# Optimization experiments

Hardware: AMD Instinct MI355X
Metric: run time of the kernel (lower is better)

Reference implementation:

```python
import jax, jax.numpy as jnp
import numpy as np

T = 2048        # Tmax encoder frames
EPROJS = 1024   # encoder projection dim (Henc)
DUNITS = 512    # prediction net hidden
EMBED = 512     # embedding dim
JOINT = 512     # joint space dim
ODIM = 10000    # output vocab
BLANK = 0


def setup_inputs() -> dict:
    key = jax.random.key(0)
    ks = jax.random.split(key, 11)
    def g(k, shape, scale):
        return (jax.random.normal(k, shape, dtype=jnp.float32) * scale)
    inp = {
        'h': jax.random.normal(ks[0], (T, EPROJS), dtype=jnp.float32),
        # Embedding with padding_idx=blank -> blank row zeroed
        'embed': g(ks[1], (ODIM, EMBED), 0.05).at[BLANK].set(0.0),
        # LSTMCell params (torch gate order: i, f, g, o)
        'W_ih': g(ks[2], (4 * DUNITS, EMBED), 1.0 / np.sqrt(EMBED)),
        'W_hh': g(ks[3], (4 * DUNITS, DUNITS), 1.0 / np.sqrt(DUNITS)),
        'b_ih': g(ks[4], (4 * DUNITS,), 0.01),
        'b_hh': g(ks[5], (4 * DUNITS,), 0.01),
        # joint network
        'W_enc': g(ks[6], (JOINT, EPROJS), 1.0 / np.sqrt(EPROJS)),
        'b_enc': g(ks[7], (JOINT,), 0.01),
        'W_dec': g(ks[8], (JOINT, DUNITS), 1.0 / np.sqrt(DUNITS)),  # no bias
        'W_out': g(ks[9], (ODIM, JOINT), 1.0 / np.sqrt(JOINT)),
        'b_out': g(ks[10], (ODIM,), 0.01),
    }
    return inp


def _lstm_cell(x, h_prev, c_prev, W_ih, W_hh, b_ih, b_hh):
    gates = W_ih @ x + b_ih + W_hh @ h_prev + b_hh  # (4*DUNITS,)
    i, f, g, o = jnp.split(gates, 4)
    c = jax.nn.sigmoid(f) * c_prev + jax.nn.sigmoid(i) * jnp.tanh(g)
    h = jax.nn.sigmoid(o) * jnp.tanh(c)
    return h, c


def reference(h, embed, W_ih, W_hh, b_ih, b_hh, W_enc, b_enc, W_dec, W_out, b_out):
    # Precompute encoder-side joint projection (same math, hoisted out of loop)
    h_proj = h @ W_enc.T + b_enc  # (T, JOINT)

    # Initial prediction-net step on zero embedding from zero state
    zeros_e = jnp.zeros((EMBED,), dtype=h.dtype)
    zeros_d = jnp.zeros((DUNITS,), dtype=h.dtype)
    y0, c0 = _lstm_cell(zeros_e, zeros_d, zeros_d, W_ih, W_hh, b_ih, b_hh)

    def step(carry, hp_t):
        y, c, score = carry
        # joint: tanh(lin_enc(h_t) + lin_dec(y)) -> lin_out -> log_softmax
        ytu = jax.nn.log_softmax(W_out @ jnp.tanh(hp_t + W_dec @ y) + b_out)
        logp = jnp.max(ytu)
        pred = jnp.argmax(ytu)
        emitted = pred != BLANK
        # Candidate prediction-net update with embedded token
        ey = embed[pred]
        y_new, c_new = _lstm_cell(ey, y, c, W_ih, W_hh, b_ih, b_hh)
        y = jnp.where(emitted, y_new, y)
        c = jnp.where(emitted, c_new, c)
        score = score + jnp.where(emitted, logp, jnp.zeros_like(logp))
        tok = jnp.where(emitted, pred, BLANK).astype(jnp.int32)
        return (y, c, score), tok

    (y, c, score), yseq = jax.lax.scan(step, (y0, c0, jnp.float32(0.0)), h_proj)
    # yseq: (T,) int32, BLANK where no symbol was emitted at that frame
    return yseq, score
```

## Files before the change

kernel.cpp:

```cpp
#include <hip/hip_runtime.h>
#include <stdint.h>

typedef unsigned long long u64;
typedef uint32_t u32;

#define NB     256
#define NT     256
#define TMAX   2048
#define EPROJS 1024
#define DUNITS 512
#define EMBED  512
#define JOINT  512
#define ODIM   10000

#define N_LSTM 32
#define CONS0  32
#define N_CONS 223
#define AGG_B  255
#define MAGIC  0xD07ED07Eu

#define WS_PK   0
#define WS_SA   7168
#define WS_DN   14336
#define WS_Y    15360
#define WS_U    23552
#define WS_HP   32768

__device__ __forceinline__ float aloadf(const float* p){
  return __hip_atomic_load(p, __ATOMIC_RELAXED, __HIP_MEMORY_SCOPE_AGENT);
}
__device__ __forceinline__ void astoref(float* p, float v){
  __hip_atomic_store(p, v, __ATOMIC_RELAXED, __HIP_MEMORY_SCOPE_AGENT);
}
__device__ __forceinline__ u64 aloadu64(const u64* p){
  return __hip_atomic_load(p, __ATOMIC_RELAXED, __HIP_MEMORY_SCOPE_AGENT);
}
__device__ __forceinline__ void astoreu64(u64* p, u64 v){
  __hip_atomic_store(p, v, __ATOMIC_RELAXED, __HIP_MEMORY_SCOPE_AGENT);
}
__device__ __forceinline__ u32 aloadu32(const u32* p){
  return __hip_atomic_load(p, __ATOMIC_RELAXED, __HIP_MEMORY_SCOPE_AGENT);
}
__device__ __forceinline__ void astoreu32(u32* p, u32 v){
  __hip_atomic_store(p, v, __ATOMIC_RELAXED, __HIP_MEMORY_SCOPE_AGENT);
}

__device__ __forceinline__ u32 ordbits(float f){
  u32 u = __float_as_uint(f);
  return (u & 0x80000000u) ? ~u : (u | 0x80000000u);
}
__device__ __forceinline__ float unordbits(u32 o){
  u32 u = (o & 0x80000000u) ? (o & 0x7fffffffu) : ~o;
  return __uint_as_float(u);
}
__device__ __forceinline__ float sigmoidf_(float x){ return 1.0f/(1.0f+expf(-x)); }

__device__ __forceinline__ float wredsum(float v){
  #pragma unroll
  for (int o=32;o>0;o>>=1) v += __shfl_xor(v, o);
  return v;
}
__device__ __forceinline__ u64 wredmax64(u64 v){
  #pragma unroll
  for (int o=32;o>0;o>>=1){ u64 x = __shfl_xor(v, o); v = (x>v)?x:v; }
  return v;
}

__device__ __forceinline__ int zslot(int j){
  return (j&7)*64 + ((j>>3) ^ ((j&7)<<2));
}

#define LOAD8(dst, baseptr) { const float4* _p=(const float4*)(baseptr); \
  float4 _a=_p[0], _b=_p[1]; \
  dst[0]=_a.x; dst[1]=_a.y; dst[2]=_a.z; dst[3]=_a.w; \
  dst[4]=_b.x; dst[5]=_b.y; dst[6]=_b.z; dst[7]=_b.w; }

__global__ void rnnt_init(char* ws){
  u32* p = (u32*)ws;
  for (int i = threadIdx.x; i < 8192; i += blockDim.x) p[i] = 0u;
}

__global__ void __launch_bounds__(NT, 1)
rnnt_decode(const float* __restrict__ h,    const float* __restrict__ embed,
            const float* __restrict__ W_ih, const float* __restrict__ W_hh,
            const float* __restrict__ b_ih, const float* __restrict__ b_hh,
            const float* __restrict__ W_enc,const float* __restrict__ b_enc,
            const float* __restrict__ W_dec,const float* __restrict__ W_out,
            const float* __restrict__ b_out,
            float* __restrict__ out, char* __restrict__ ws)
{
  const int b    = blockIdx.x;
  const int tid  = threadIdx.x;
  const int lane = tid & 63;
  const int w    = tid >> 6;

  u64*  ytag  = (u64*)(ws + WS_Y);
  u64*  utag  = (u64*)(ws + WS_U);
  u64*  pkall = (u64*)(ws + WS_PK);
  u64*  saall = (u64*)(ws + WS_SA);
  u32*  done  = (u32*)(ws + WS_DN);
  float* hp   = (float*)(ws + WS_HP);

  __shared__ float smem[8192];
  float* PL = smem;
  float* GL = &smem[4416];
  u64*   R64= (u64*)&smem[4480];
  float* RF = &smem[4488];
  float* ZL = &smem[4544];

  {
    float (*lds_h)[EPROJS] = (float(*)[EPROJS])smem;
    #pragma unroll
    for (int r=0;r<8;r++){
      const float4 hv = *(const float4*)(h + (size_t)(8*b + r)*EPROJS + tid*4);
      *(float4*)&lds_h[r][tid*4] = hv;
    }
    __syncthreads();
    for (int p=0;p<2;p++){
      const int j = p*NT + tid;
      float acc[8] = {0,0,0,0,0,0,0,0};
      const float4* wrow = (const float4*)(W_enc + (size_t)j*EPROJS);
      for (int k4=0;k4<EPROJS/4;k4++){
        const float4 wv = wrow[k4];
        #pragma unroll
        for (int t8=0;t8<8;t8++){
          const float4 hv = *(const float4*)&lds_h[t8][k4*4];
          acc[t8] = fmaf(wv.x,hv.x, fmaf(wv.y,hv.y, fmaf(wv.z,hv.z, fmaf(wv.w,hv.w, acc[t8]))));
        }
      }
      const float be = b_enc[j];
      #pragma unroll
      for (int t8=0;t8<8;t8++)
        astoref(&hp[(size_t)(8*b+t8)*JOINT + j], acc[t8] + be);
    }
    asm volatile("s_waitcnt vmcnt(0)" ::: "memory");
    if (tid==0) astoreu32(&done[b], MAGIC);
    __syncthreads();
  }

  if (b < N_LSTM){
    const int d = b;
    float wih[16][8], whh[16][8];
    #pragma unroll
    for (int q=0;q<16;q++){
      const int gr = w*DUNITS + 16*d + q;
      LOAD8(wih[q], W_ih + (size_t)gr*EMBED  + lane*8);
      LOAD8(whh[q], W_hh + (size_t)gr*DUNITS + lane*8);
    }
    float wdr[4][8];
    #pragma unroll
    for (int i=0;i<4;i++){
      const int r = 16*d + 4*w + i;
      LOAD8(wdr[i], W_dec + (size_t)r*DUNITS + 8*lane);
    }
    float bias_r = 0.0f;
    if (tid < 64){
      const int gr = (tid>>4)*DUNITS + 16*d + (tid&15);
      bias_r = b_ih[gr] + b_hh[gr];
    }
    float c_st = 0.0f, y_st = 0.0f;
    if (tid < 16){
      const int j = 16*d + tid;
      const float gi = b_ih[j]            + b_hh[j];
      const float gg = b_ih[2*DUNITS + j] + b_hh[2*DUNITS + j];
      const float go = b_ih[3*DUNITS + j] + b_hh[3*DUNITS + j];
      c_st = sigmoidf_(gi)*tanhf(gg);
      y_st = sigmoidf_(go)*tanhf(c_st);
      astoreu64(&ytag[512 + j], ((u64)1u<<32) | (u64)__float_as_uint(y_st));
    }

    for (int t=0;t<TMAX;t++){
      const u32 g = (u32)(t+1);
      const u64* yb = ytag + (size_t)(g&1)*512;
      u64 yv[8];
      for(;;){
        bool ok = true;
        #pragma unroll
        for (int i=0;i<8;i++){
          yv[i] = aloadu64(&yb[8*lane + i]);
          ok &= ((u32)(yv[i]>>32) == g);
        }
        if (ok) break;
      }
      float y8[8];
      #pragma unroll
      for (int i=0;i<8;i++) y8[i] = __uint_as_float((u32)yv[i]);
      {
        float p0=0.f,p1=0.f,p2=0.f,p3=0.f;
        #pragma unroll
        for (int k=0;k<8;k++){
          p0 = fmaf(wdr[0][k], y8[k], p0);
          p1 = fmaf(wdr[1][k], y8[k], p1);
          p2 = fmaf(wdr[2][k], y8[k], p2);
          p3 = fmaf(wdr[3][k], y8[k], p3);
        }
        #pragma unroll
        for (int o=32;o>0;o>>=1){
          p0 += __shfl_xor(p0,o); p1 += __shfl_xor(p1,o);
          p2 += __shfl_xor(p2,o); p3 += __shfl_xor(p3,o);
        }
        if (lane < 4){
          const float pv = (lane==0)?p0:(lane==1)?p1:(lane==2)?p2:p3;
          astoreu64(&utag[(size_t)(g&1)*512 + 16*d + 4*w + lane],
                    ((u64)g<<32) | (u64)__float_as_uint(pv));
        }
      }
      float vp[16];
      #pragma unroll
      for (int q=0;q<16;q++){
        float a=0.f;
        #pragma unroll
        for (int k=0;k<8;k++) a = fmaf(whh[q][k], y8[k], a);
        vp[q] = a;
      }
      u64 pk = 0;
      {
        const u64* pks = pkall + (g&3)*224;
        for(;;){
          pk = (tid < N_CONS) ? aloadu64(&pks[tid]) : 0;
          const int ok = (tid < N_CONS) ? ((u32)(pk>>48) >= g) : 1;
          if (__all(ok)) break;
        }
      }
      const u64 m = wredmax64(pk);
      if (lane==0) R64[w] = m;
      const int predw = (int)((~(u32)m) & 0xFFFFu);
      float e8[8];
      LOAD8(e8, embed + (size_t)predw*EMBED + 8*lane);
      __syncthreads();
      u64 best = R64[0];
      #pragma unroll
      for (int i=1;i<4;i++){ const u64 x=R64[i]; best = (x>best)?x:best; }
      const int pred = (int)((~(u32)best) & 0xFFFFu);
      const int emitted = (pred != 0);
      if (m != best){
        LOAD8(e8, embed + (size_t)pred*EMBED + 8*lane);
      }
      #pragma unroll
      for (int q=0;q<16;q++){
        float a = vp[q];
        #pragma unroll
        for (int k=0;k<8;k++) a = fmaf(wih[q][k], e8[k], a);
        PL[(w*16+q)*68 + lane] = a;
      }
      __syncthreads();
      if (tid < 64){
        const float* row = &PL[tid*68];
        float s = bias_r;
        #pragma unroll
        for (int k4=0;k4<16;k4++){
          const float4 v4 = *(const float4*)&row[4*k4];
          s += v4.x + v4.y + v4.z + v4.w;
        }
        GL[tid] = s;
      }
      __syncthreads();
      if (tid < 16){
        const float gi=GL[tid], gf=GL[16+tid], gg=GL[32+tid], go=GL[48+tid];
        const float cn = sigmoidf_(gf)*c_st + sigmoidf_(gi)*tanhf(gg);
        const float yn = sigmoidf_(go)*tanhf(cn);
        if (emitted){ c_st = cn; y_st = yn; }
        if (t < TMAX-1)
          astoreu64(&ytag[(size_t)((g+1)&1)*512 + 16*d + tid],
                    ((u64)(g+1)<<32) | (u64)__float_as_uint(y_st));
      }
    }
  }
  else if (b < AGG_B){
    const int cb = b - CONS0;
    int rowstart, rowcnt;
    if (cb < 188){ rowstart = cb*45;                 rowcnt = 45; }
    else         { rowstart = 8460 + (cb-188)*44;    rowcnt = 44; }
    float wout[12][8];
    #pragma unroll
    for (int q=0;q<12;q++){
      const int s = 12*w + q;
      if (s < rowcnt){
        LOAD8(wout[q], W_out + (size_t)(rowstart+s)*JOINT + lane*8);
      } else {
        #pragma unroll
        for (int k=0;k<8;k++) wout[q][k]=0.f;
      }
    }
    float my_bo = 0.f; int my_row = 0; bool my_val = false;
    if (tid < rowcnt){ my_val = true; my_row = rowstart + tid; my_bo = b_out[my_row]; }

    for(;;){
      const u32 dv = aloadu32(&done[tid]);
      if (__all(dv == MAGIC)) break;
    }
    __syncthreads();

    const int j0 = 2*tid, j1 = 2*tid+1;
    const int s0 = zslot(j0), s1 = zslot(j1);
    for (int t=0;t<TMAX;t++){
      const u32 g = (u32)(t+1);
      const float2 h2 = *(const float2*)(hp + (size_t)t*JOINT + j0);
      const u64* ub = utag + (size_t)(g&1)*512;
      u64 ua, ub2;
      for(;;){
        ua  = aloadu64(&ub[j0]);
        ub2 = aloadu64(&ub[j1]);
        if ( (((u32)(ua>>32))==g) & (((u32)(ub2>>32))==g) ) break;
      }
      ZL[s0] = tanhf(h2.x + __uint_as_float((u32)ua));
      ZL[s1] = tanhf(h2.y + __uint_as_float((u32)ub2));
      __syncthreads();
      float z8[8];
      #pragma unroll
      for (int e=0;e<8;e++) z8[e] = ZL[e*64 + (lane ^ (e<<2))];
      #pragma unroll
      for (int q=0;q<12;q++){
        float a=0.f;
        #pragma unroll
        for (int k=0;k<8;k++) a = fmaf(wout[q][k], z8[k], a);
        PL[(12*w+q)*68 + lane] = a;
      }
      __syncthreads();
      u64 key = 0; float lg = 0.f;
      if (tid < 48){
        const float* row = &PL[tid*68];
        float s = my_bo;
        #pragma unroll
        for (int k4=0;k4<16;k4++){
          const float4 v4 = *(const float4*)&row[4*k4];
          s += v4.x + v4.y + v4.z + v4.w;
        }
        lg = s;
        if (my_val) key = ((u64)ordbits(lg)<<16) | (u64)(0xFFFFu & ~(u32)my_row);
      }
      if (w == 0){
        const u64 bk = wredmax64(key);
        const float mw = unordbits((u32)(bk>>16));
        const float e  = my_val ? __expf(lg - mw) : 0.f;
        const float sw = wredsum(e);
        if (lane == 0){
          astoreu64(&saall[(g&3)*224 + cb], ((u64)g<<32) | (u64)__float_as_uint(sw));
          astoreu64(&pkall[(g&3)*224 + cb], ((u64)g<<48) | bk);
        }
      }
    }
  }
  else {
    float score = 0.0f;
    for (int t=0;t<TMAX;t++){
      const u32 g = (u32)(t+1);
      const u64* pks = pkall + (g&3)*224;
      const u64* sas = saall + (g&3)*224;
      u64 pk=0, sa=0;
      for(;;){
        if (tid < N_CONS){ pk = aloadu64(&pks[tid]); sa = aloadu64(&sas[tid]); }
        const int ok = (tid < N_CONS) ? (((u32)(pk>>48)==g) & (((u32)(sa>>32))==g)) : 1;
        if (__all(ok)) break;
      }
      { u64 m = wredmax64(pk); if (lane==0) R64[w]=m; }
      __syncthreads();
      u64 best = R64[0];
      #pragma unroll
      for (int i=1;i<4;i++){ const u64 x=R64[i]; best = (x>best)?x:best; }
      const float mstar = unordbits((u32)(best>>16));
      float term = (tid < N_CONS) ?
        __uint_as_float((u32)sa) * __expf(unordbits((u32)(pk>>16)) - mstar) : 0.f;
      term = wredsum(term);
      if (lane==0) RF[w] = term;
      __syncthreads();
      if (tid==0){
        const float S = RF[0]+RF[1]+RF[2]+RF[3];
        const int pred = (int)((~(u32)best) & 0xFFFFu);
        if (pred != 0) score += -logf(S);
        out[t] = (float)pred;
      }
      __syncthreads();
    }
    if (tid==0) out[TMAX] = score;
  }
}

extern "C" void kernel_launch(void* const* d_in, const int* in_sizes, int n_in,
                              void* d_out, int out_size, void* d_ws, size_t ws_size,
                              hipStream_t stream)
{
  const float* h     = (const float*)d_in[0];
  const float* embed = (const float*)d_in[1];
  const float* W_ih  = (const float*)d_in[2];
  const float* W_hh  = (const float*)d_in[3];
  const float* b_ih  = (const float*)d_in[4];
  const float* b_hh  = (const float*)d_in[5];
  const float* W_enc = (const float*)d_in[6];
  const float* b_enc = (const float*)d_in[7];
  const float* W_dec = (const float*)d_in[8];
  const float* W_out = (const float*)d_in[9];
  const float* b_out = (const float*)d_in[10];
  float* out = (float*)d_out;
  char* ws = (char*)d_ws;

  hipLaunchKernelGGL(rnnt_init, dim3(1), dim3(NT), 0, stream, ws);
  hipLaunchKernelGGL(rnnt_decode, dim3(NB), dim3(NT), 0, stream,
                     h, embed, W_ih, W_hh, b_ih, b_hh, W_enc, b_enc, W_dec, W_out, b_out,
                     out, ws);
}
```

Baseline: 19.73 ms.

## Precompute W_dec partial projections in LSTM blocks and add spin backoff with flow control

```diff
diff --git a/kernel.cpp b/kernel.cpp
--- a/kernel.cpp
+++ b/kernel.cpp
@@ -22,9 +22,11 @@
 #define WS_PK   0
 #define WS_SA   7168
 #define WS_DN   14336
-#define WS_Y    15360
-#define WS_U    23552
-#define WS_HP   32768
+#define WS_AGG  15360
+#define WS_Y    16384
+#define WS_U    20480
+#define WS_PART 24576
+#define WS_HP   155648
 
 __device__ __forceinline__ float aloadf(const float* p){
   return __hip_atomic_load(p, __ATOMIC_RELAXED, __HIP_MEMORY_SCOPE_AGENT);
@@ -77,7 +79,8 @@
 
 __global__ void rnnt_init(char* ws){
   u32* p = (u32*)ws;
-  for (int i = threadIdx.x; i < 8192; i += blockDim.x) p[i] = 0u;
+  const int stride = blockDim.x * gridDim.x;
+  for (int i = blockIdx.x*blockDim.x + threadIdx.x; i < 38912; i += stride) p[i] = 0u;
 }
 
 __global__ void __launch_bounds__(NT, 1)
@@ -96,9 +99,11 @@
 
   u64*  ytag  = (u64*)(ws + WS_Y);
   u64*  utag  = (u64*)(ws + WS_U);
+  u64*  ptag  = (u64*)(ws + WS_PART);
   u64*  pkall = (u64*)(ws + WS_PK);
   u64*  saall = (u64*)(ws + WS_SA);
   u32*  done  = (u32*)(ws + WS_DN);
+  u32*  aggr  = (u32*)(ws + WS_AGG);
   float* hp   = (float*)(ws + WS_HP);
 
   __shared__ float smem[8192];
@@ -106,7 +111,9 @@
   float* GL = &smem[4416];
   u64*   R64= (u64*)&smem[4480];
   float* RF = &smem[4488];
+  float* YO = &smem[4492];
   float* ZL = &smem[4544];
+  float* PS = &smem[5056];
 
   {
     float (*lds_h)[EPROJS] = (float(*)[EPROJS])smem;
@@ -147,11 +154,17 @@
       LOAD8(wih[q], W_ih + (size_t)gr*EMBED  + lane*8);
       LOAD8(whh[q], W_hh + (size_t)gr*DUNITS + lane*8);
     }
-    float wdr[4][8];
-    #pragma unroll
-    for (int i=0;i<4;i++){
-      const int r = 16*d + 4*w + i;
-      LOAD8(wdr[i], W_dec + (size_t)r*DUNITS + 8*lane);
+    float wdc0[16], wdc1[16];
+    {
+      const float4* p0 = (const float4*)(W_dec + (size_t)(2*tid)*DUNITS   + 16*d);
+      const float4* p1 = (const float4*)(W_dec + (size_t)(2*tid+1)*DUNITS + 16*d);
+      #pragma unroll
+      for (int k4=0;k4<4;k4++){
+        const float4 a = p0[k4];
+        wdc0[4*k4+0]=a.x; wdc0[4*k4+1]=a.y; wdc0[4*k4+2]=a.z; wdc0[4*k4+3]=a.w;
+        const float4 c = p1[k4];
+        wdc1[4*k4+0]=c.x; wdc1[4*k4+1]=c.y; wdc1[4*k4+2]=c.z; wdc1[4*k4+3]=c.w;
+      }
     }
     float bias_r = 0.0f;
     if (tid < 64){
@@ -166,44 +179,46 @@
       const float go = b_ih[3*DUNITS + j] + b_hh[3*DUNITS + j];
       c_st = sigmoidf_(gi)*tanhf(gg);
       y_st = sigmoidf_(go)*tanhf(c_st);
-      astoreu64(&ytag[512 + j], ((u64)1u<<32) | (u64)__float_as_uint(y_st));
-    }
-
+      YO[tid] = y_st;
+      astoreu64(&ytag[j], ((u64)1u<<32) | (u64)__float_as_uint(y_st));
+    }
+    __syncthreads();
+    {
+      float p0=0.f, p1=0.f;
+      #pragma unroll
+      for (int k=0;k<16;k++){ p0 = fmaf(wdc0[k], YO[k], p0); p1 = fmaf(wdc1[k], YO[k], p1); }
+      u64* up = ptag + (size_t)d*512;
+      astoreu64(&up[2*tid],   ((u64)1u<<32) | (u64)__float_as_uint(p0));
+      astoreu64(&up[2*tid+1], ((u64)1u<<32) | (u64)__float_as_uint(p1));
+    }
+
+    const int jj = tid & 15;
+    const int pp = tid >> 4;
     for (int t=0;t<TMAX;t++){
       const u32 g = (u32)(t+1);
-      const u64* yb = ytag + (size_t)(g&1)*512;
-      u64 yv[8];
+      u64 pv0, pv1, yv[8];
       for(;;){
-        bool ok = true;
+        pv0 = aloadu64(&ptag[(size_t)(2*pp)*512   + 16*d + jj]);
+        pv1 = aloadu64(&ptag[(size_t)(2*pp+1)*512 + 16*d + jj]);
+        bool ok = ((u32)(pv0>>32)==g) & ((u32)(pv1>>32)==g);
         #pragma unroll
         for (int i=0;i<8;i++){
-          yv[i] = aloadu64(&yb[8*lane + i]);
+          yv[i] = aloadu64(&ytag[8*lane + i]);
           ok &= ((u32)(yv[i]>>32) == g);
         }
         if (ok) break;
+        __builtin_amdgcn_s_sleep(1);
       }
       float y8[8];
       #pragma unroll
       for (int i=0;i<8;i++) y8[i] = __uint_as_float((u32)yv[i]);
-      {
-        float p0=0.f,p1=0.f,p2=0.f,p3=0.f;
-        #pragma unroll
-        for (int k=0;k<8;k++){
-          p0 = fmaf(wdr[0][k], y8[k], p0);
-          p1 = fmaf(wdr[1][k], y8[k], p1);
-          p2 = fmaf(wdr[2][k], y8[k], p2);
-          p3 = fmaf(wdr[3][k], y8[k], p3);
-        }
-        #pragma unroll
-        for (int o=32;o>0;o>>=1){
-          p0 += __shfl_xor(p0,o); p1 += __shfl_xor(p1,o);
-          p2 += __shfl_xor(p2,o); p3 += __shfl_xor(p3,o);
-        }
-        if (lane < 4){
-          const float pv = (lane==0)?p0:(lane==1)?p1:(lane==2)?p2:p3;
-          astoreu64(&utag[(size_t)(g&1)*512 + 16*d + 4*w + lane],
-                    ((u64)g<<32) | (u64)__float_as_uint(pv));
-        }
+      PS[jj*17 + pp] = __uint_as_float((u32)pv0) + __uint_as_float((u32)pv1);
+      __syncthreads();
+      if (tid < 16){
+        float s = 0.f;
+        #pragma unroll
+        for (int k=0;k<16;k++) s += PS[tid*17 + k];
+        astoreu64(&utag[16*d + tid], ((u64)g<<32) | (u64)__float_as_uint(s));
       }
       float vp[16];
       #pragma unroll
@@ -220,6 +235,7 @@
           pk = (tid < N_CONS) ? aloadu64(&pks[tid]) : 0;
           const int ok = (tid < N_CONS) ? ((u32)(pk>>48) >= g) : 1;
           if (__all(ok)) break;
+          __builtin_amdgcn_s_sleep(1);
         }
       }
       const u64 m = wredmax64(pk);
@@ -260,9 +276,18 @@
         const float cn = sigmoidf_(gf)*c_st + sigmoidf_(gi)*tanhf(gg);
         const float yn = sigmoidf_(go)*tanhf(cn);
         if (emitted){ c_st = cn; y_st = yn; }
+        YO[tid] = y_st;
         if (t < TMAX-1)
-          astoreu64(&ytag[(size_t)((g+1)&1)*512 + 16*d + tid],
-                    ((u64)(g+1)<<32) | (u64)__float_as_uint(y_st));
+          astoreu64(&ytag[16*d + tid], ((u64)(g+1)<<32) | (u64)__float_as_uint(y_st));
+      }
+      __syncthreads();
+      if (t < TMAX-1){
+        float p0=0.f, p1=0.f;
+        #pragma unroll
+        for (int k=0;k<16;k++){ p0 = fmaf(wdc0[k], YO[k], p0); p1 = fmaf(wdc1[k], YO[k], p1); }
+        u64* up = ptag + (size_t)d*512;
+        astoreu64(&up[2*tid],   ((u64)(g+1)<<32) | (u64)__float_as_uint(p0));
+        astoreu64(&up[2*tid+1], ((u64)(g+1)<<32) | (u64)__float_as_uint(p1));
       }
     }
   }
@@ -284,10 +309,12 @@
     }
     float my_bo = 0.f; int my_row = 0; bool my_val = false;
     if (tid < rowcnt){ my_val = true; my_row = rowstart + tid; my_bo = b_out[my_row]; }
+    const u32* agrep = &aggr[(cb&7)*32];
 
     for(;;){
       const u32 dv = aloadu32(&done[tid]);
       if (__all(dv == MAGIC)) break;
+      __builtin_amdgcn_s_sleep(2);
     }
     __syncthreads();
 
@@ -296,12 +323,12 @@
     for (int t=0;t<TMAX;t++){
       const u32 g = (u32)(t+1);
       const float2 h2 = *(const float2*)(hp + (size_t)t*JOINT + j0);
-      const u64* ub = utag + (size_t)(g&1)*512;
       u64 ua, ub2;
       for(;;){
-        ua  = aloadu64(&ub[j0]);
-        ub2 = aloadu64(&ub[j1]);
+        ua  = aloadu64(&utag[j0]);
+        ub2 = aloadu64(&utag[j1]);
         if ( (((u32)(ua>>32))==g) & (((u32)(ub2>>32))==g) ) break;
+        __builtin_amdgcn_s_sleep(1);
       }
       ZL[s0] = tanhf(h2.x + __uint_as_float((u32)ua));
       ZL[s1] = tanhf(h2.y + __uint_as_float((u32)ub2));
@@ -335,6 +362,7 @@
         const float e  = my_val ? __expf(lg - mw) : 0.f;
         const float sw = wredsum(e);
         if (lane == 0){
+          while ((int)(g - aloadu32(agrep)) > 3) __builtin_amdgcn_s_sleep(2);
           astoreu64(&saall[(g&3)*224 + cb], ((u64)g<<32) | (u64)__float_as_uint(sw));
           astoreu64(&pkall[(g&3)*224 + cb], ((u64)g<<48) | bk);
         }
@@ -352,6 +380,7 @@
         if (tid < N_CONS){ pk = aloadu64(&pks[tid]); sa = aloadu64(&sas[tid]); }
         const int ok = (tid < N_CONS) ? (((u32)(pk>>48)==g) & (((u32)(sa>>32))==g)) : 1;
         if (__all(ok)) break;
+        __builtin_amdgcn_s_sleep(2);
       }
       { u64 m = wredmax64(pk); if (lane==0) R64[w]=m; }
       __syncthreads();
@@ -371,6 +400,7 @@
         out[t] = (float)pred;
       }
       __syncthreads();
+      if (tid < 8) astoreu32(&aggr[tid*32], g);
     }
     if (tid==0) out[TMAX] = score;
   }
@@ -394,7 +424,7 @@
   float* out = (float*)d_out;
   char* ws = (char*)d_ws;
 
-  hipLaunchKernelGGL(rnnt_init, dim3(1), dim3(NT), 0, stream, ws);
+  hipLaunchKernelGGL(rnnt_init, dim3(32), dim3(NT), 0, stream, ws);
   hipLaunchKernelGGL(rnnt_decode, dim3(NB), dim3(NT), 0, stream,
                      h, embed, W_ih, W_hh, b_ih, b_hh, W_enc, b_enc, W_dec, W_out, b_out,
                      out, ws);
```

New measurement: 17.70 ms. 1.11x faster.

## Single-buffer y/u tags with monotonic tag checks and aggregator backpressure

Applied to the files above, without the earlier changes.

```diff
diff --git a/kernel.cpp b/kernel.cpp
--- a/kernel.cpp
+++ b/kernel.cpp
@@ -22,9 +22,10 @@
 #define WS_PK   0
 #define WS_SA   7168
 #define WS_DN   14336
-#define WS_Y    15360
-#define WS_U    23552
-#define WS_HP   32768
+#define WS_AGG  15360
+#define WS_Y    16384
+#define WS_U    20480
+#define WS_HP   24576
 
 __device__ __forceinline__ float aloadf(const float* p){
   return __hip_atomic_load(p, __ATOMIC_RELAXED, __HIP_MEMORY_SCOPE_AGENT);
@@ -77,7 +78,8 @@
 
 __global__ void rnnt_init(char* ws){
   u32* p = (u32*)ws;
-  for (int i = threadIdx.x; i < 8192; i += blockDim.x) p[i] = 0u;
+  const int stride = blockDim.x * gridDim.x;
+  for (int i = blockIdx.x*blockDim.x + threadIdx.x; i < 6144; i += stride) p[i] = 0u;
 }
 
 __global__ void __launch_bounds__(NT, 1)
@@ -94,11 +96,12 @@
   const int lane = tid & 63;
   const int w    = tid >> 6;
 
-  u64*  ytag  = (u64*)(ws + WS_Y);
-  u64*  utag  = (u64*)(ws + WS_U);
+  u64*   ytag = (u64*)(ws + WS_Y);
+  u64*   utag = (u64*)(ws + WS_U);
   u64*  pkall = (u64*)(ws + WS_PK);
   u64*  saall = (u64*)(ws + WS_SA);
   u32*  done  = (u32*)(ws + WS_DN);
+  u32*  aggr  = (u32*)(ws + WS_AGG);
   float* hp   = (float*)(ws + WS_HP);
 
   __shared__ float smem[8192];
@@ -106,7 +109,7 @@
   float* GL = &smem[4416];
   u64*   R64= (u64*)&smem[4480];
   float* RF = &smem[4488];
-  float* ZL = &smem[4544];
+  float* SL = &smem[4544];
 
   {
     float (*lds_h)[EPROJS] = (float(*)[EPROJS])smem;
@@ -166,25 +169,23 @@
       const float go = b_ih[3*DUNITS + j] + b_hh[3*DUNITS + j];
       c_st = sigmoidf_(gi)*tanhf(gg);
       y_st = sigmoidf_(go)*tanhf(c_st);
-      astoreu64(&ytag[512 + j], ((u64)1u<<32) | (u64)__float_as_uint(y_st));
+      astoreu64(&ytag[j], ((u64)1u<<32) | (u64)__float_as_uint(y_st));
     }
 
     for (int t=0;t<TMAX;t++){
       const u32 g = (u32)(t+1);
-      const u64* yb = ytag + (size_t)(g&1)*512;
-      u64 yv[8];
-      for(;;){
-        bool ok = true;
-        #pragma unroll
-        for (int i=0;i<8;i++){
-          yv[i] = aloadu64(&yb[8*lane + i]);
-          ok &= ((u32)(yv[i]>>32) == g);
-        }
-        if (ok) break;
+      {
+        u64 ya, yb;
+        for(;;){
+          ya = aloadu64(&ytag[2*tid]); yb = aloadu64(&ytag[2*tid+1]);
+          const int ok = ((u32)(ya>>32)>=g) & ((u32)(yb>>32)>=g);
+          if (__syncthreads_and(ok)) break;
+        }
       }
       float y8[8];
       #pragma unroll
-      for (int i=0;i<8;i++) y8[i] = __uint_as_float((u32)yv[i]);
+      for (int i=0;i<8;i++)
+        y8[i] = __uint_as_float((u32)aloadu64(&ytag[8*lane + i]));
       {
         float p0=0.f,p1=0.f,p2=0.f,p3=0.f;
         #pragma unroll
@@ -201,7 +202,7 @@
         }
         if (lane < 4){
           const float pv = (lane==0)?p0:(lane==1)?p1:(lane==2)?p2:p3;
-          astoreu64(&utag[(size_t)(g&1)*512 + 16*d + 4*w + lane],
+          astoreu64(&utag[16*d + 4*w + lane],
                     ((u64)g<<32) | (u64)__float_as_uint(pv));
         }
       }
@@ -214,13 +215,10 @@
         vp[q] = a;
       }
       u64 pk = 0;
-      {
-        const u64* pks = pkall + (g&3)*224;
-        for(;;){
-          pk = (tid < N_CONS) ? aloadu64(&pks[tid]) : 0;
-          const int ok = (tid < N_CONS) ? ((u32)(pk>>48) >= g) : 1;
-          if (__all(ok)) break;
-        }
+      for(;;){
+        if (tid < N_CONS) pk = aloadu64(&pkall[(g&3)*224 + tid]);
+        const int ok = (tid < N_CONS) ? ((u32)(pk>>48) >= g) : 1;
+        if (__syncthreads_and(ok)) break;
       }
       const u64 m = wredmax64(pk);
       if (lane==0) R64[w] = m;
@@ -261,8 +259,7 @@
         const float yn = sigmoidf_(go)*tanhf(cn);
         if (emitted){ c_st = cn; y_st = yn; }
         if (t < TMAX-1)
-          astoreu64(&ytag[(size_t)((g+1)&1)*512 + 16*d + tid],
-                    ((u64)(g+1)<<32) | (u64)__float_as_uint(y_st));
+          astoreu64(&ytag[16*d + tid], ((u64)(g+1)<<32) | (u64)__float_as_uint(y_st));
       }
     }
   }
@@ -284,31 +281,31 @@
     }
     float my_bo = 0.f; int my_row = 0; bool my_val = false;
     if (tid < rowcnt){ my_val = true; my_row = rowstart + tid; my_bo = b_out[my_row]; }
+    const u32* agrep = &aggr[(cb&7)*32];
 
     for(;;){
-      const u32 dv = aloadu32(&done[tid]);
-      if (__all(dv == MAGIC)) break;
-    }
-    __syncthreads();
+      const int ok = (aloadu32(&done[tid]) == MAGIC);
+      if (__syncthreads_and(ok)) break;
+    }
 
     const int j0 = 2*tid, j1 = 2*tid+1;
     const int s0 = zslot(j0), s1 = zslot(j1);
     for (int t=0;t<TMAX;t++){
       const u32 g = (u32)(t+1);
       const float2 h2 = *(const float2*)(hp + (size_t)t*JOINT + j0);
-      const u64* ub = utag + (size_t)(g&1)*512;
       u64 ua, ub2;
       for(;;){
-        ua  = aloadu64(&ub[j0]);
-        ub2 = aloadu64(&ub[j1]);
-        if ( (((u32)(ua>>32))==g) & (((u32)(ub2>>32))==g) ) break;
-      }
-      ZL[s0] = tanhf(h2.x + __uint_as_float((u32)ua));
-      ZL[s1] = tanhf(h2.y + __uint_as_float((u32)ub2));
+        ua  = aloadu64(&utag[j0]);
+        ub2 = aloadu64(&utag[j1]);
+        const int ok = (((u32)(ua>>32))>=g) & (((u32)(ub2>>32))>=g);
+        if (__syncthreads_and(ok)) break;
+      }
+      SL[s0] = tanhf(h2.x + __uint_as_float((u32)ua));
+      SL[s1] = tanhf(h2.y + __uint_as_float((u32)ub2));
       __syncthreads();
       float z8[8];
       #pragma unroll
-      for (int e=0;e<8;e++) z8[e] = ZL[e*64 + (lane ^ (e<<2))];
+      for (int e=0;e<8;e++) z8[e] = SL[e*64 + (lane ^ (e<<2))];
       #pragma unroll
       for (int q=0;q<12;q++){
         float a=0.f;
@@ -335,6 +332,7 @@
         const float e  = my_val ? __expf(lg - mw) : 0.f;
         const float sw = wredsum(e);
         if (lane == 0){
+          while ((int)(g - aloadu32(agrep)) > 3) __builtin_amdgcn_s_sleep(2);
           astoreu64(&saall[(g&3)*224 + cb], ((u64)g<<32) | (u64)__float_as_uint(sw));
           astoreu64(&pkall[(g&3)*224 + cb], ((u64)g<<48) | bk);
         }
@@ -351,7 +349,7 @@
       for(;;){
         if (tid < N_CONS){ pk = aloadu64(&pks[tid]); sa = aloadu64(&sas[tid]); }
         const int ok = (tid < N_CONS) ? (((u32)(pk>>48)==g) & (((u32)(sa>>32))==g)) : 1;
-        if (__all(ok)) break;
+        if (__syncthreads_and(ok)) break;
       }
       { u64 m = wredmax64(pk); if (lane==0) R64[w]=m; }
       __syncthreads();
@@ -371,6 +369,7 @@
         out[t] = (float)pred;
       }
       __syncthreads();
+      if (tid < 8) astoreu32(&aggr[tid*32], g);
     }
     if (tid==0) out[TMAX] = score;
   }
@@ -394,7 +393,7 @@
   float* out = (float*)d_out;
   char* ws = (char*)d_ws;
 
-  hipLaunchKernelGGL(rnnt_init, dim3(1), dim3(NT), 0, stream, ws);
+  hipLaunchKernelGGL(rnnt_init, dim3(32), dim3(NT), 0, stream, ws);
   hipLaunchKernelGGL(rnnt_decode, dim3(NB), dim3(NT), 0, stream,
                      h, embed, W_ih, W_hh, b_ih, b_hh, W_enc, b_enc, W_dec, W_out, b_out,
                      out, ws);
```

After: 21.37 ms. 8.3% more time.
